# Kernel optimization log

Measured on AMD Instinct MI355X. Metric: run time of the kernel, lower is better.

## Reference

```python
import jax, jax.numpy as jnp
import numpy as np
from jax import lax

# Problem constants (match input_specs / init_kwargs)
B, N, F_IN = 16, 4096, 64          # clouds, points per cloud, feature dim
RATIO, R, K = 0.25, 0.1, 64        # fps ratio, ball radius, max neighbors
S = int(N * RATIO)                 # sampled centers per cloud (1024)
H1, H2, OUT = 64, 64, 128          # MLP [F_IN+3 -> 64 -> 64 -> 128]


def _fps(pos):
    """Farthest point sampling on one cloud. pos: [N,3] -> idx [S] (start at 0)."""
    def step(carry, _):
        mind, last = carry
        d = jnp.sum((pos - pos[last]) ** 2, axis=-1)
        mind = jnp.minimum(mind, d)
        nxt = jnp.argmax(mind)
        return (mind, nxt), nxt
    init = (jnp.full((pos.shape[0],), jnp.inf, pos.dtype), jnp.array(0))
    _, rest = lax.scan(step, init, None, length=S - 1)
    return jnp.concatenate([jnp.zeros((1,), rest.dtype), rest])


def _mlp(h, W1, b1, W2, b2, W3, b3):
    h = jax.nn.relu(h @ W1 + b1)
    h = jax.nn.relu(h @ W2 + b2)
    return jax.nn.relu(h @ W3 + b3)


def setup_inputs() -> dict:
    key = jax.random.key(0)
    ks = jax.random.split(key, 8)
    x = jax.random.normal(ks[0], (B * N, F_IN), jnp.float32)
    pos = jax.random.uniform(ks[1], (B * N, 3), jnp.float32)  # unit cube
    batch = jnp.arange(B * N, dtype=jnp.int64) // N           # cloud ids, equal-size clouds
    d_in = F_IN + 3
    W1 = jax.random.normal(ks[2], (d_in, H1), jnp.float32) / np.sqrt(d_in)
    b1 = jnp.zeros((H1,), jnp.float32)
    W2 = jax.random.normal(ks[3], (H1, H2), jnp.float32) / np.sqrt(H1)
    b2 = jnp.zeros((H2,), jnp.float32)
    W3 = jax.random.normal(ks[4], (H2, OUT), jnp.float32) / np.sqrt(H2)
    b3 = jnp.zeros((OUT,), jnp.float32)
    return {"x": x, "pos": pos, "batch": batch,
            "W1": W1, "b1": b1, "W2": W2, "b2": b2, "W3": W3, "b3": b3}


def reference(x, pos, batch, W1, b1, W2, b2, W3, b3):
    xb = x.reshape(B, N, F_IN)
    pb = pos.reshape(B, N, 3)
    # --- fps(pos, batch, ratio) : per-cloud farthest point sampling ---
    idx = jax.vmap(_fps)(pb)                                   # [B,S]
    pos_s = jnp.take_along_axis(pb, idx[:, :, None], axis=1)   # [B,S,3]
    # --- radius(pos, pos[idx], r, max_num_neighbors=K) : ball query ---
    d2 = jnp.sum((pos_s[:, :, None, :] - pb[:, None, :, :]) ** 2, axis=-1)  # [B,S,N]
    neg = jnp.where(d2 <= R * R, -d2, -jnp.inf)
    vals, nbr = lax.top_k(neg, K)                              # [B,S,K] nearest-in-ball
    valid = jnp.isfinite(vals)                                 # center is its own neighbor -> >=1 valid
    # --- PointNetConv: msg = nn(concat(x_j, pos_j - pos_i)), max aggregation ---
    x_j = jax.vmap(lambda a, i: a[i])(xb, nbr)                 # [B,S,K,F_IN]
    p_j = jax.vmap(lambda a, i: a[i])(pb, nbr)                 # [B,S,K,3]
    msg = jnp.concatenate([x_j, p_j - pos_s[:, :, None, :]], axis=-1)
    m = _mlp(msg, W1, b1, W2, b2, W3, b3)                      # [B,S,K,OUT]
    m = jnp.where(valid[..., None], m, -jnp.inf)
    out = jnp.max(m, axis=2)                                   # [B,S,OUT]
    batch_s = jnp.take_along_axis(batch.reshape(B, N), idx, axis=1).reshape(-1)
    return out.reshape(B * S, OUT), pos_s.reshape(B * S, 3), batch_s
```

## Files before the change

kernel.cpp:

```cpp
#include <hip/hip_runtime.h>
#include <hip/hip_bf16.h>
#include <math.h>


#define NB 16
#define NP 4096
#define FIN 64
#define NS 1024
#define KN 64
#define CAP 256
#define CPB 8

typedef __attribute__((ext_vector_type(8))) short bf16x8;
typedef __attribute__((ext_vector_type(4))) float f32x4;

__device__ __forceinline__ float dist2e(float ax, float ay, float az,
                                        float bx, float by, float bz) {
    float dx = __fsub_rn(ax, bx);
    float dy = __fsub_rn(ay, by);
    float dz = __fsub_rn(az, bz);
    return __fadd_rn(__fadd_rn(__fmul_rn(dx, dx), __fmul_rn(dy, dy)),
                     __fmul_rn(dz, dz));
}

__device__ __forceinline__ short f2bf(float f) {
    unsigned u = __float_as_uint(f);
    unsigned r = (u + 0x7FFFu + ((u >> 16) & 1u)) >> 16;
    return (short)r;
}

#define DPP_KEY_MAX(k, CTRL)                                                   \
    do {                                                                       \
        int _lo = (int)(unsigned)((k) & 0xFFFFFFFFull);                        \
        int _hi = (int)(unsigned)((k) >> 32);                                  \
        int _plo = __builtin_amdgcn_update_dpp(_lo, _lo, CTRL, 0xF, 0xF, false);\
        int _phi = __builtin_amdgcn_update_dpp(_hi, _hi, CTRL, 0xF, 0xF, false);\
        unsigned long long _nk =                                               \
            ((unsigned long long)(unsigned)_phi << 32) | (unsigned)_plo;       \
        if (_nk > (k)) (k) = _nk;                                              \
    } while (0)

__global__ __launch_bounds__(256) void fps_kernel(const float* __restrict__ pos,
                                                  int* __restrict__ fps_idx,
                                                  float* __restrict__ out_pos,
                                                  float* __restrict__ out_batch) {
    const int b = blockIdx.x;
    const int tid = threadIdx.x;
    const int wv = tid >> 6;
    __shared__ __align__(16) float4 hist[NS];
    __shared__ __align__(16) float bc[2][4][8];
    const float* p = pos + (size_t)b * NP * 3;
    float lx[16], ly[16], lz[16], md[16];
#pragma unroll
    for (int i = 0; i < 16; ++i) {
        int j = tid + (i << 8);
        lx[i] = p[j * 3 + 0];
        ly[i] = p[j * 3 + 1];
        lz[i] = p[j * 3 + 2];
        md[i] = INFINITY;
    }
    const float c0x = p[0], c0y = p[1], c0z = p[2];
    float cx = c0x, cy = c0y, cz = c0z;
    for (int s = 1; s < NS; ++s) {
        float bv = -1.0f;
        int bi = 0;
        float wx = 0.f, wy = 0.f, wz = 0.f;
#pragma unroll
        for (int i = 0; i < 16; ++i) {
            float d = dist2e(lx[i], ly[i], lz[i], cx, cy, cz);
            float m = md[i];
            m = d < m ? d : m;
            md[i] = m;
            bool take = (m > bv);
            bv = take ? m : bv;
            bi = take ? (tid + (i << 8)) : bi;
            wx = take ? lx[i] : wx;
            wy = take ? ly[i] : wy;
            wz = take ? lz[i] : wz;
        }
        unsigned long long key =
            ((unsigned long long)__float_as_uint(bv) << 32) |
            (unsigned)(~(unsigned)bi);
        const unsigned long long my = key;
        DPP_KEY_MAX(key, 0x111);
        DPP_KEY_MAX(key, 0x112);
        DPP_KEY_MAX(key, 0x114);
        DPP_KEY_MAX(key, 0x118);
        DPP_KEY_MAX(key, 0x142);
        DPP_KEY_MAX(key, 0x143);
        const unsigned kwlo =
            (unsigned)__builtin_amdgcn_readlane((int)(unsigned)(key & 0xFFFFFFFFull), 63);
        const unsigned kwhi =
            (unsigned)__builtin_amdgcn_readlane((int)(unsigned)(key >> 32), 63);
        const unsigned long long kw = ((unsigned long long)kwhi << 32) | kwlo;
        const int buf = s & 1;
        if (my == kw) {
            bc[buf][wv][0] = __uint_as_float(kwlo);
            bc[buf][wv][1] = __uint_as_float(kwhi);
            bc[buf][wv][2] = wx;
            bc[buf][wv][3] = wy;
            bc[buf][wv][4] = wz;
        }
        __syncthreads();
        unsigned long long bk;
        float bx, by, bz;
        {
            float4 e = *(const float4*)&bc[buf][0][0];
            bk = ((unsigned long long)__float_as_uint(e.y) << 32) |
                 __float_as_uint(e.x);
            bx = e.z; by = e.w; bz = bc[buf][0][4];
        }
#pragma unroll
        for (int w = 1; w < 4; ++w) {
            float4 e = *(const float4*)&bc[buf][w][0];
            unsigned long long k2 =
                ((unsigned long long)__float_as_uint(e.y) << 32) |
                __float_as_uint(e.x);
            float z2 = bc[buf][w][4];
            bool take = (k2 > bk);
            bk = take ? k2 : bk;
            bx = take ? e.z : bx;
            by = take ? e.w : by;
            bz = take ? z2 : bz;
        }
        const int cur = (int)(~(unsigned)(bk & 0xFFFFFFFFull));
        cx = bx; cy = by; cz = bz;
        if (tid == 0) hist[s] = make_float4(__int_as_float(cur), bx, by, bz);
    }
    __syncthreads();
    for (int s = tid; s < NS; s += 256) {
        if (s == 0) {
            fps_idx[b * NS] = 0;
            out_pos[(size_t)(b * NS) * 3 + 0] = c0x;
            out_pos[(size_t)(b * NS) * 3 + 1] = c0y;
            out_pos[(size_t)(b * NS) * 3 + 2] = c0z;
        } else {
            float4 e = hist[s];
            fps_idx[b * NS + s] = __float_as_int(e.x);
            out_pos[(size_t)(b * NS + s) * 3 + 0] = e.y;
            out_pos[(size_t)(b * NS + s) * 3 + 1] = e.z;
            out_pos[(size_t)(b * NS + s) * 3 + 2] = e.w;
        }
        out_batch[b * NS + s] = (float)b;
    }
}

__global__ __launch_bounds__(256) void ball_kernel(const float* __restrict__ pos,
                                                   const int* __restrict__ fps_idx,
                                                   int* __restrict__ nbr_cnt,
                                                   int* __restrict__ nbr_idx) {
    __shared__ float px[NP], py[NP], pz[NP];
    __shared__ float cd2[4][CAP];
    __shared__ int cix[4][CAP];
    const int tid = threadIdx.x;
    const int wv = tid >> 6, lane = tid & 63;
    const int b = blockIdx.x >> 4;
    const int grp = blockIdx.x & 15;
    const float* p = pos + (size_t)b * NP * 3;
    for (int e = tid; e < NP; e += 256) {
        px[e] = p[e * 3 + 0];
        py[e] = p[e * 3 + 1];
        pz[e] = p[e * 3 + 2];
    }
    __syncthreads();
    for (int i = 0; i < 16; ++i) {
        const int s = grp * 64 + i * 4 + wv;
        const int cen = b * NS + s;
        const int ci = fps_idx[cen];
        const float cx = px[ci], cy = py[ci], cz = pz[ci];
        int cnt = 0;
        for (int it = 0; it < NP / 64; ++it) {
            const int j = it * 64 + lane;
            float d2 = dist2e(cx, cy, cz, px[j], py[j], pz[j]);
            bool in = (d2 <= 0.01f);
            unsigned long long m = __ballot(in);
            if (in) {
                int slot = cnt + __popcll(m & ((1ull << lane) - 1ull));
                if (slot < CAP) { cd2[wv][slot] = d2; cix[wv][slot] = j; }
            }
            cnt += __popcll(m);
        }
        if (cnt > CAP) cnt = CAP;
        const int keep = cnt <= KN ? cnt : KN;
        if (lane == 0) nbr_cnt[cen] = keep;
        if (cnt <= KN) {
            if (lane < cnt) nbr_idx[(size_t)cen * KN + lane] = cix[wv][lane];
        } else {
            for (int e = lane; e < cnt; e += 64) {
                float d = cd2[wv][e];
                int id = cix[wv][e];
                int rank = 0;
                for (int q = 0; q < cnt; ++q) {
                    float dq = cd2[wv][q];
                    int iq = cix[wv][q];
                    rank += (dq < d || (dq == d && iq < id)) ? 1 : 0;
                }
                if (rank < KN) nbr_idx[(size_t)cen * KN + rank] = id;
            }
        }
    }
}

__global__ __launch_bounds__(256) void conv_kernel(const float* __restrict__ pos,
                                                   const float* __restrict__ x,
                                                   const int* __restrict__ fps_idx,
                                                   const int* __restrict__ nbr_cnt,
                                                   const int* __restrict__ nbr_idx,
                                                   const float* __restrict__ W1,
                                                   const float* __restrict__ b1,
                                                   const float* __restrict__ W2,
                                                   const float* __restrict__ b2,
                                                   const float* __restrict__ W3,
                                                   const float* __restrict__ b3,
                                                   float* __restrict__ out) {
    const int tid = threadIdx.x;
    const int lane = tid & 63;
    const int w = tid >> 6;
    const int lg = lane >> 4;
    const int lr = lane & 15;
    __shared__ short h1s[64 * 64];
    __shared__ short h2s[64 * 64];
    __shared__ float dpx[64], dpy[64], dpz[64];
    __shared__ int jr[64];
    __shared__ float omax[4][128];
    bf16x8 w1f[3][4], w2f[2][4], w3f[2][8];
#pragma unroll
    for (int kt = 0; kt < 3; ++kt)
#pragma unroll
        for (int ct = 0; ct < 4; ++ct) {
            bf16x8 f;
#pragma unroll
            for (int i = 0; i < 8; ++i) {
                int k = 32 * kt + 8 * lg + i;
                float v = (k < 67) ? W1[k * 64 + 16 * ct + lr] : 0.f;
                f[i] = f2bf(v);
            }
            w1f[kt][ct] = f;
        }
#pragma unroll
    for (int kt = 0; kt < 2; ++kt)
#pragma unroll
        for (int ct = 0; ct < 4; ++ct) {
            bf16x8 f;
#pragma unroll
            for (int i = 0; i < 8; ++i) {
                int k = 32 * kt + 8 * lg + i;
                f[i] = f2bf(W2[k * 64 + 16 * ct + lr]);
            }
            w2f[kt][ct] = f;
        }
#pragma unroll
    for (int kt = 0; kt < 2; ++kt)
#pragma unroll
        for (int ct = 0; ct < 8; ++ct) {
            bf16x8 f;
#pragma unroll
            for (int i = 0; i < 8; ++i) {
                int k = 32 * kt + 8 * lg + i;
                f[i] = f2bf(W3[k * 128 + 16 * ct + lr]);
            }
            w3f[kt][ct] = f;
        }
    float b1v[4], b2v[4], b3v[8];
#pragma unroll
    for (int ct = 0; ct < 4; ++ct) { b1v[ct] = b1[16 * ct + lr]; b2v[ct] = b2[16 * ct + lr]; }
#pragma unroll
    for (int ct = 0; ct < 8; ++ct) b3v[ct] = b3[16 * ct + lr];

    for (int cc = 0; cc < CPB; ++cc) {
        const int cen = blockIdx.x * CPB + cc;
        const int b = cen >> 10;
        const int C = nbr_cnt[cen];
        if (tid < 64) {
            const float* pb = pos + (size_t)b * NP * 3;
            const int ci = fps_idx[cen];
            const float cx = pb[ci * 3 + 0], cy = pb[ci * 3 + 1], cz = pb[ci * 3 + 2];
            if (tid < C) {
                int j = nbr_idx[(size_t)cen * KN + tid];
                jr[tid] = b * NP + j;
                dpx[tid] = pb[j * 3 + 0] - cx;
                dpy[tid] = pb[j * 3 + 1] - cy;
                dpz[tid] = pb[j * 3 + 2] - cz;
            } else {
                jr[tid] = b * NP;
                dpx[tid] = 0.f; dpy[tid] = 0.f; dpz[tid] = 0.f;
            }
        }
        __syncthreads();
        const int arow = 16 * w + lr;
        bf16x8 a0, a1, a2;
        {
            const float* xr = x + (size_t)jr[arow] * FIN + 8 * lg;
            float4 v0 = *(const float4*)(xr + 0);
            float4 v1 = *(const float4*)(xr + 4);
            float4 v2 = *(const float4*)(xr + 32);
            float4 v3 = *(const float4*)(xr + 36);
            a0[0] = f2bf(v0.x); a0[1] = f2bf(v0.y); a0[2] = f2bf(v0.z); a0[3] = f2bf(v0.w);
            a0[4] = f2bf(v1.x); a0[5] = f2bf(v1.y); a0[6] = f2bf(v1.z); a0[7] = f2bf(v1.w);
            a1[0] = f2bf(v2.x); a1[1] = f2bf(v2.y); a1[2] = f2bf(v2.z); a1[3] = f2bf(v2.w);
            a1[4] = f2bf(v3.x); a1[5] = f2bf(v3.y); a1[6] = f2bf(v3.z); a1[7] = f2bf(v3.w);
            float d0 = (lg == 0) ? dpx[arow] : 0.f;
            float d1 = (lg == 0) ? dpy[arow] : 0.f;
            float d2 = (lg == 0) ? dpz[arow] : 0.f;
            a2[0] = f2bf(d0); a2[1] = f2bf(d1); a2[2] = f2bf(d2);
            a2[3] = 0; a2[4] = 0; a2[5] = 0; a2[6] = 0; a2[7] = 0;
        }
        {
            f32x4 acc[4];
#pragma unroll
            for (int ct = 0; ct < 4; ++ct) {
                acc[ct] = (f32x4){b1v[ct], b1v[ct], b1v[ct], b1v[ct]};
                acc[ct] = __builtin_amdgcn_mfma_f32_16x16x32_bf16(a0, w1f[0][ct], acc[ct], 0, 0, 0);
                acc[ct] = __builtin_amdgcn_mfma_f32_16x16x32_bf16(a1, w1f[1][ct], acc[ct], 0, 0, 0);
                acc[ct] = __builtin_amdgcn_mfma_f32_16x16x32_bf16(a2, w1f[2][ct], acc[ct], 0, 0, 0);
            }
#pragma unroll
            for (int ct = 0; ct < 4; ++ct)
#pragma unroll
                for (int r = 0; r < 4; ++r) {
                    int rw = 16 * w + 4 * lg + r;
                    int idx = rw * 64 + 16 * ct + lr;
                    h1s[idx ^ ((rw & 7) << 3)] = f2bf(fmaxf(acc[ct][r], 0.f));
                }
        }
        bf16x8 ha0 = *(bf16x8*)&h1s[(arow * 64 + 0  + 8 * lg) ^ ((arow & 7) << 3)];
        bf16x8 ha1 = *(bf16x8*)&h1s[(arow * 64 + 32 + 8 * lg) ^ ((arow & 7) << 3)];
        {
            f32x4 acc[4];
#pragma unroll
            for (int ct = 0; ct < 4; ++ct) {
                acc[ct] = (f32x4){b2v[ct], b2v[ct], b2v[ct], b2v[ct]};
                acc[ct] = __builtin_amdgcn_mfma_f32_16x16x32_bf16(ha0, w2f[0][ct], acc[ct], 0, 0, 0);
                acc[ct] = __builtin_amdgcn_mfma_f32_16x16x32_bf16(ha1, w2f[1][ct], acc[ct], 0, 0, 0);
            }
#pragma unroll
            for (int ct = 0; ct < 4; ++ct)
#pragma unroll
                for (int r = 0; r < 4; ++r) {
                    int rw = 16 * w + 4 * lg + r;
                    int idx = rw * 64 + 16 * ct + lr;
                    h2s[idx ^ ((rw & 7) << 3)] = f2bf(fmaxf(acc[ct][r], 0.f));
                }
        }
        bf16x8 hb0 = *(bf16x8*)&h2s[(arow * 64 + 0  + 8 * lg) ^ ((arow & 7) << 3)];
        bf16x8 hb1 = *(bf16x8*)&h2s[(arow * 64 + 32 + 8 * lg) ^ ((arow & 7) << 3)];
        {
            f32x4 acc3[8];
#pragma unroll
            for (int ct = 0; ct < 8; ++ct) {
                acc3[ct] = (f32x4){b3v[ct], b3v[ct], b3v[ct], b3v[ct]};
                acc3[ct] = __builtin_amdgcn_mfma_f32_16x16x32_bf16(hb0, w3f[0][ct], acc3[ct], 0, 0, 0);
                acc3[ct] = __builtin_amdgcn_mfma_f32_16x16x32_bf16(hb1, w3f[1][ct], acc3[ct], 0, 0, 0);
            }
#pragma unroll
            for (int ct = 0; ct < 8; ++ct) {
                float m = -INFINITY;
#pragma unroll
                for (int r = 0; r < 4; ++r) {
                    int rg = 16 * w + 4 * lg + r;
                    float v = fmaxf(acc3[ct][r], 0.f);
                    m = (rg < C && v > m) ? v : m;
                }
                m = fmaxf(m, __shfl_xor(m, 16, 64));
                m = fmaxf(m, __shfl_xor(m, 32, 64));
                if (lg == 0) omax[w][16 * ct + lr] = m;
            }
        }
        __syncthreads();
        if (tid < 128) {
            float m = fmaxf(fmaxf(omax[0][tid], omax[1][tid]),
                            fmaxf(omax[2][tid], omax[3][tid]));
            out[(size_t)cen * 128 + tid] = m;
        }
        __syncthreads();
    }
}

extern "C" void kernel_launch(void* const* d_in, const int* in_sizes, int n_in,
                              void* d_out, int out_size, void* d_ws, size_t ws_size,
                              hipStream_t stream) {
    const float* x   = (const float*)d_in[0];
    const float* pos = (const float*)d_in[1];
    const float* W1  = (const float*)d_in[3];
    const float* b1  = (const float*)d_in[4];
    const float* W2  = (const float*)d_in[5];
    const float* b2  = (const float*)d_in[6];
    const float* W3  = (const float*)d_in[7];
    const float* b3  = (const float*)d_in[8];
    float* out = (float*)d_out;
    char* ws = (char*)d_ws;
    int* fps_idx = (int*)(ws);
    int* nbr_cnt = (int*)(ws + 16384 * 4);
    int* nbr_idx = (int*)(ws + 16384 * 8);
    float* out_feat  = out;
    float* out_pos   = out + (size_t)16384 * 128;
    float* out_batch = out + (size_t)16384 * 131;
    fps_kernel<<<NB, 256, 0, stream>>>(pos, fps_idx, out_pos, out_batch);
    ball_kernel<<<NB * 16, 256, 0, stream>>>(pos, fps_idx, nbr_cnt, nbr_idx);
    conv_kernel<<<NB * NS / CPB, 256, 0, stream>>>(pos, x, fps_idx, nbr_cnt,
                                                   nbr_idx, W1, b1, W2, b2,
                                                   W3, b3, out_feat);
}
```

Measured before the change: 1.141 ms.

## Fuse FPS, ball query and conv into one persistent kernel with progress flags

Replaces the three sequential kernels with one persistent launch. Sixteen blocks run farthest point sampling and publish sampled centers to global memory every 64 steps behind a release/acquire progress counter. The other 240 blocks spin on those counters and do the ball query and MLP max-aggregation for centers already produced, so neighbor search and convolution overlap the serial FPS. This relies on all 256 blocks being co-resident, adds spin-wait and fence overhead, and lowers the candidate cap to 128 while reading positions from global memory instead of shared memory.

```diff
diff --git a/kernel.cpp b/kernel.cpp
--- a/kernel.cpp
+++ b/kernel.cpp
@@ -8,8 +8,9 @@
 #define FIN 64
 #define NS 1024
 #define KN 64
-#define CAP 256
-#define CPB 8
+#define CAP 128
+#define NCONS 240
+#define NCHUNK 4096
 
 typedef __attribute__((ext_vector_type(8))) short bf16x8;
 typedef __attribute__((ext_vector_type(4))) float f32x4;
@@ -40,339 +41,361 @@
         if (_nk > (k)) (k) = _nk;                                              \
     } while (0)
 
-__global__ __launch_bounds__(256) void fps_kernel(const float* __restrict__ pos,
-                                                  int* __restrict__ fps_idx,
-                                                  float* __restrict__ out_pos,
-                                                  float* __restrict__ out_batch) {
-    const int b = blockIdx.x;
+#define SMEM_BYTES 27648
+
+__global__ __launch_bounds__(256) void fused_kernel(
+        const float* __restrict__ pos, const float* __restrict__ x,
+        const float* __restrict__ W1, const float* __restrict__ b1,
+        const float* __restrict__ W2, const float* __restrict__ b2,
+        const float* __restrict__ W3, const float* __restrict__ b3,
+        float* __restrict__ out_feat, float* __restrict__ out_pos,
+        float* __restrict__ out_batch, float* __restrict__ histg,
+        int* __restrict__ progress) {
+    __shared__ __align__(16) char smem[SMEM_BYTES];
     const int tid = threadIdx.x;
+    const int lane = tid & 63;
     const int wv = tid >> 6;
-    __shared__ __align__(16) float4 hist[NS];
-    __shared__ __align__(16) float bc[2][4][8];
-    const float* p = pos + (size_t)b * NP * 3;
-    float lx[16], ly[16], lz[16], md[16];
-#pragma unroll
-    for (int i = 0; i < 16; ++i) {
-        int j = tid + (i << 8);
-        lx[i] = p[j * 3 + 0];
-        ly[i] = p[j * 3 + 1];
-        lz[i] = p[j * 3 + 2];
-        md[i] = INFINITY;
-    }
-    const float c0x = p[0], c0y = p[1], c0z = p[2];
-    float cx = c0x, cy = c0y, cz = c0z;
-    for (int s = 1; s < NS; ++s) {
-        float bv = -1.0f;
-        int bi = 0;
-        float wx = 0.f, wy = 0.f, wz = 0.f;
+
+    if (blockIdx.x < NB) {
+        const int b = blockIdx.x;
+        float4* hist = (float4*)smem;
+        float (*bc)[4][8] = (float(*)[4][8])(smem + 16384);
+        const float* p = pos + (size_t)b * NP * 3;
+        float lx[16], ly[16], lz[16], md[16];
 #pragma unroll
         for (int i = 0; i < 16; ++i) {
-            float d = dist2e(lx[i], ly[i], lz[i], cx, cy, cz);
-            float m = md[i];
-            m = d < m ? d : m;
-            md[i] = m;
-            bool take = (m > bv);
-            bv = take ? m : bv;
-            bi = take ? (tid + (i << 8)) : bi;
-            wx = take ? lx[i] : wx;
-            wy = take ? ly[i] : wy;
-            wz = take ? lz[i] : wz;
-        }
-        unsigned long long key =
-            ((unsigned long long)__float_as_uint(bv) << 32) |
-            (unsigned)(~(unsigned)bi);
-        const unsigned long long my = key;
-        DPP_KEY_MAX(key, 0x111);
-        DPP_KEY_MAX(key, 0x112);
-        DPP_KEY_MAX(key, 0x114);
-        DPP_KEY_MAX(key, 0x118);
-        DPP_KEY_MAX(key, 0x142);
-        DPP_KEY_MAX(key, 0x143);
-        const unsigned kwlo =
-            (unsigned)__builtin_amdgcn_readlane((int)(unsigned)(key & 0xFFFFFFFFull), 63);
-        const unsigned kwhi =
-            (unsigned)__builtin_amdgcn_readlane((int)(unsigned)(key >> 32), 63);
-        const unsigned long long kw = ((unsigned long long)kwhi << 32) | kwlo;
-        const int buf = s & 1;
-        if (my == kw) {
-            bc[buf][wv][0] = __uint_as_float(kwlo);
-            bc[buf][wv][1] = __uint_as_float(kwhi);
-            bc[buf][wv][2] = wx;
-            bc[buf][wv][3] = wy;
-            bc[buf][wv][4] = wz;
+            int j = tid + (i << 8);
+            lx[i] = p[j * 3 + 0];
+            ly[i] = p[j * 3 + 1];
+            lz[i] = p[j * 3 + 2];
+            md[i] = INFINITY;
+        }
+        const float c0x = p[0], c0y = p[1], c0z = p[2];
+        float cx = c0x, cy = c0y, cz = c0z;
+        if (tid == 0) hist[0] = make_float4(0.f, c0x, c0y, c0z);
+        for (int s = 1; s < NS; ++s) {
+            float bv = -1.0f;
+            int bi = 0;
+            float wx = 0.f, wy = 0.f, wz = 0.f;
+#pragma unroll
+            for (int i = 0; i < 16; ++i) {
+                float d = dist2e(lx[i], ly[i], lz[i], cx, cy, cz);
+                float m = md[i];
+                m = d < m ? d : m;
+                md[i] = m;
+                bool take = (m > bv);
+                bv = take ? m : bv;
+                bi = take ? (tid + (i << 8)) : bi;
+                wx = take ? lx[i] : wx;
+                wy = take ? ly[i] : wy;
+                wz = take ? lz[i] : wz;
+            }
+            unsigned long long key =
+                ((unsigned long long)__float_as_uint(bv) << 32) |
+                (unsigned)(~(unsigned)bi);
+            const unsigned long long my = key;
+            DPP_KEY_MAX(key, 0x111);
+            DPP_KEY_MAX(key, 0x112);
+            DPP_KEY_MAX(key, 0x114);
+            DPP_KEY_MAX(key, 0x118);
+            DPP_KEY_MAX(key, 0x142);
+            DPP_KEY_MAX(key, 0x143);
+            const unsigned kwlo = (unsigned)__builtin_amdgcn_readlane(
+                (int)(unsigned)(key & 0xFFFFFFFFull), 63);
+            const unsigned kwhi = (unsigned)__builtin_amdgcn_readlane(
+                (int)(unsigned)(key >> 32), 63);
+            const unsigned long long kw =
+                ((unsigned long long)kwhi << 32) | kwlo;
+            const int buf = s & 1;
+            if (my == kw) {
+                bc[buf][wv][0] = __uint_as_float(kwlo);
+                bc[buf][wv][1] = __uint_as_float(kwhi);
+                bc[buf][wv][2] = wx;
+                bc[buf][wv][3] = wy;
+                bc[buf][wv][4] = wz;
+            }
+            __syncthreads();
+            if ((s & 63) == 0) {
+                const int base = s - 64;
+                if (tid < 192) {
+                    int cc = tid / 3, comp = tid % 3;
+                    float4 h = hist[base + cc];
+                    float v = comp == 0 ? h.y : (comp == 1 ? h.z : h.w);
+                    __hip_atomic_store(
+                        (unsigned*)&histg[((size_t)(b * NS + base + cc)) * 3 + comp],
+                        __float_as_uint(v), __ATOMIC_RELAXED,
+                        __HIP_MEMORY_SCOPE_AGENT);
+                }
+                __threadfence();
+                __syncthreads();
+                if (tid == 0)
+                    __hip_atomic_store(&progress[b], s, __ATOMIC_RELEASE,
+                                       __HIP_MEMORY_SCOPE_AGENT);
+            }
+            unsigned long long bk;
+            float bx, by, bz;
+            {
+                float4 e = *(const float4*)&bc[buf][0][0];
+                bk = ((unsigned long long)__float_as_uint(e.y) << 32) |
+                     __float_as_uint(e.x);
+                bx = e.z; by = e.w; bz = bc[buf][0][4];
+            }
+#pragma unroll
+            for (int w = 1; w < 4; ++w) {
+                float4 e = *(const float4*)&bc[buf][w][0];
+                unsigned long long k2 =
+                    ((unsigned long long)__float_as_uint(e.y) << 32) |
+                    __float_as_uint(e.x);
+                float z2 = bc[buf][w][4];
+                bool take = (k2 > bk);
+                bk = take ? k2 : bk;
+                bx = take ? e.z : bx;
+                by = take ? e.w : by;
+                bz = take ? z2 : bz;
+            }
+            const int cur = (int)(~(unsigned)(bk & 0xFFFFFFFFull));
+            cx = bx; cy = by; cz = bz;
+            if (tid == 0)
+                hist[s] = make_float4(__int_as_float(cur), bx, by, bz);
         }
         __syncthreads();
-        unsigned long long bk;
-        float bx, by, bz;
-        {
-            float4 e = *(const float4*)&bc[buf][0][0];
-            bk = ((unsigned long long)__float_as_uint(e.y) << 32) |
-                 __float_as_uint(e.x);
-            bx = e.z; by = e.w; bz = bc[buf][0][4];
-        }
-#pragma unroll
-        for (int w = 1; w < 4; ++w) {
-            float4 e = *(const float4*)&bc[buf][w][0];
-            unsigned long long k2 =
-                ((unsigned long long)__float_as_uint(e.y) << 32) |
-                __float_as_uint(e.x);
-            float z2 = bc[buf][w][4];
-            bool take = (k2 > bk);
-            bk = take ? k2 : bk;
-            bx = take ? e.z : bx;
-            by = take ? e.w : by;
-            bz = take ? z2 : bz;
-        }
-        const int cur = (int)(~(unsigned)(bk & 0xFFFFFFFFull));
-        cx = bx; cy = by; cz = bz;
-        if (tid == 0) hist[s] = make_float4(__int_as_float(cur), bx, by, bz);
-    }
-    __syncthreads();
-    for (int s = tid; s < NS; s += 256) {
-        if (s == 0) {
-            fps_idx[b * NS] = 0;
-            out_pos[(size_t)(b * NS) * 3 + 0] = c0x;
-            out_pos[(size_t)(b * NS) * 3 + 1] = c0y;
-            out_pos[(size_t)(b * NS) * 3 + 2] = c0z;
-        } else {
+        if (tid < 192) {
+            int cc = tid / 3, comp = tid % 3;
+            float4 h = hist[960 + cc];
+            float v = comp == 0 ? h.y : (comp == 1 ? h.z : h.w);
+            __hip_atomic_store(
+                (unsigned*)&histg[((size_t)(b * NS + 960 + cc)) * 3 + comp],
+                __float_as_uint(v), __ATOMIC_RELAXED, __HIP_MEMORY_SCOPE_AGENT);
+        }
+        __threadfence();
+        __syncthreads();
+        if (tid == 0)
+            __hip_atomic_store(&progress[b], NS, __ATOMIC_RELEASE,
+                               __HIP_MEMORY_SCOPE_AGENT);
+        for (int s = tid; s < NS; s += 256) {
             float4 e = hist[s];
-            fps_idx[b * NS + s] = __float_as_int(e.x);
             out_pos[(size_t)(b * NS + s) * 3 + 0] = e.y;
             out_pos[(size_t)(b * NS + s) * 3 + 1] = e.z;
             out_pos[(size_t)(b * NS + s) * 3 + 2] = e.w;
-        }
-        out_batch[b * NS + s] = (float)b;
+            out_batch[b * NS + s] = (float)b;
+        }
+        return;
     }
-}
-
-__global__ __launch_bounds__(256) void ball_kernel(const float* __restrict__ pos,
-                                                   const int* __restrict__ fps_idx,
-                                                   int* __restrict__ nbr_cnt,
-                                                   int* __restrict__ nbr_idx) {
-    __shared__ float px[NP], py[NP], pz[NP];
-    __shared__ float cd2[4][CAP];
-    __shared__ int cix[4][CAP];
-    const int tid = threadIdx.x;
-    const int wv = tid >> 6, lane = tid & 63;
-    const int b = blockIdx.x >> 4;
-    const int grp = blockIdx.x & 15;
-    const float* p = pos + (size_t)b * NP * 3;
-    for (int e = tid; e < NP; e += 256) {
-        px[e] = p[e * 3 + 0];
-        py[e] = p[e * 3 + 1];
-        pz[e] = p[e * 3 + 2];
+
+    const int w = blockIdx.x - NB;
+    short* h1s = (short*)smem;
+    short* h2s = (short*)(smem + 8192);
+    float* cd2 = (float*)(smem + 16384);
+    int*   cix = (int*)(smem + 18432);
+    float* dpxA = (float*)(smem + 20480);
+    float* dpyA = (float*)(smem + 21504);
+    float* dpzA = (float*)(smem + 22528);
+    int*   jA   = (int*)(smem + 23552);
+    float* omax = (float*)(smem + 24576);
+    int*   keepW = (int*)(smem + 26624);
+    const int lg = lane >> 4;
+    const int lr = lane & 15;
+    bf16x8 w1f[3][4], w2f[2][4], w3f[2][8];
+#pragma unroll
+    for (int kt = 0; kt < 3; ++kt)
+#pragma unroll
+        for (int ct = 0; ct < 4; ++ct) {
+            bf16x8 f;
+#pragma unroll
+            for (int i = 0; i < 8; ++i) {
+                int k = 32 * kt + 8 * lg + i;
+                float v = (k < 67) ? W1[k * 64 + 16 * ct + lr] : 0.f;
+                f[i] = f2bf(v);
+            }
+            w1f[kt][ct] = f;
+        }
+#pragma unroll
+    for (int kt = 0; kt < 2; ++kt)
+#pragma unroll
+        for (int ct = 0; ct < 4; ++ct) {
+            bf16x8 f;
+#pragma unroll
+            for (int i = 0; i < 8; ++i) {
+                int k = 32 * kt + 8 * lg + i;
+                f[i] = f2bf(W2[k * 64 + 16 * ct + lr]);
+            }
+            w2f[kt][ct] = f;
+        }
+#pragma unroll
+    for (int kt = 0; kt < 2; ++kt)
+#pragma unroll
+        for (int ct = 0; ct < 8; ++ct) {
+            bf16x8 f;
+#pragma unroll
+            for (int i = 0; i < 8; ++i) {
+                int k = 32 * kt + 8 * lg + i;
+                f[i] = f2bf(W3[k * 128 + 16 * ct + lr]);
+            }
+            w3f[kt][ct] = f;
+        }
+    float b1v[4], b2v[4], b3v[8];
+#pragma unroll
+    for (int ct = 0; ct < 4; ++ct) {
+        b1v[ct] = b1[16 * ct + lr];
+        b2v[ct] = b2[16 * ct + lr];
     }
-    __syncthreads();
-    for (int i = 0; i < 16; ++i) {
-        const int s = grp * 64 + i * 4 + wv;
-        const int cen = b * NS + s;
-        const int ci = fps_idx[cen];
-        const float cx = px[ci], cy = py[ci], cz = pz[ci];
+#pragma unroll
+    for (int ct = 0; ct < 8; ++ct) b3v[ct] = b3[16 * ct + lr];
+
+    for (int c = w; c < NCHUNK; c += NCONS) {
+        const int s = c >> 2;
+        const int bq = (c & 3) << 2;
+        const int bw = bq + wv;
+        while (__hip_atomic_load(&progress[bw], __ATOMIC_ACQUIRE,
+                                 __HIP_MEMORY_SCOPE_AGENT) <= s) {
+            __builtin_amdgcn_s_sleep(2);
+        }
+        const size_t ho = ((size_t)(bw * NS + s)) * 3;
+        const float ccx = __uint_as_float(__hip_atomic_load(
+            (const unsigned*)&histg[ho + 0], __ATOMIC_RELAXED,
+            __HIP_MEMORY_SCOPE_AGENT));
+        const float ccy = __uint_as_float(__hip_atomic_load(
+            (const unsigned*)&histg[ho + 1], __ATOMIC_RELAXED,
+            __HIP_MEMORY_SCOPE_AGENT));
+        const float ccz = __uint_as_float(__hip_atomic_load(
+            (const unsigned*)&histg[ho + 2], __ATOMIC_RELAXED,
+            __HIP_MEMORY_SCOPE_AGENT));
         int cnt = 0;
-        for (int it = 0; it < NP / 64; ++it) {
+        const float* pcloud = pos + (size_t)bw * NP * 3;
+        for (int it = 0; it < 64; ++it) {
             const int j = it * 64 + lane;
-            float d2 = dist2e(cx, cy, cz, px[j], py[j], pz[j]);
+            const float* pp = pcloud + (size_t)j * 3;
+            float d2 = dist2e(ccx, ccy, ccz, pp[0], pp[1], pp[2]);
             bool in = (d2 <= 0.01f);
             unsigned long long m = __ballot(in);
             if (in) {
                 int slot = cnt + __popcll(m & ((1ull << lane) - 1ull));
-                if (slot < CAP) { cd2[wv][slot] = d2; cix[wv][slot] = j; }
+                if (slot < CAP) {
+                    cd2[wv * CAP + slot] = d2;
+                    cix[wv * CAP + slot] = j;
+                }
             }
             cnt += __popcll(m);
         }
         if (cnt > CAP) cnt = CAP;
         const int keep = cnt <= KN ? cnt : KN;
-        if (lane == 0) nbr_cnt[cen] = keep;
+        if (lane == 0) keepW[wv] = keep;
+        jA[wv * 64 + lane] = 0;
         if (cnt <= KN) {
-            if (lane < cnt) nbr_idx[(size_t)cen * KN + lane] = cix[wv][lane];
+            if (lane < keep) jA[wv * 64 + lane] = cix[wv * CAP + lane];
         } else {
             for (int e = lane; e < cnt; e += 64) {
-                float d = cd2[wv][e];
-                int id = cix[wv][e];
+                float d = cd2[wv * CAP + e];
+                int id = cix[wv * CAP + e];
                 int rank = 0;
                 for (int q = 0; q < cnt; ++q) {
-                    float dq = cd2[wv][q];
-                    int iq = cix[wv][q];
+                    float dq = cd2[wv * CAP + q];
+                    int iq = cix[wv * CAP + q];
                     rank += (dq < d || (dq == d && iq < id)) ? 1 : 0;
                 }
-                if (rank < KN) nbr_idx[(size_t)cen * KN + rank] = id;
-            }
-        }
-    }
-}
-
-__global__ __launch_bounds__(256) void conv_kernel(const float* __restrict__ pos,
-                                                   const float* __restrict__ x,
-                                                   const int* __restrict__ fps_idx,
-                                                   const int* __restrict__ nbr_cnt,
-                                                   const int* __restrict__ nbr_idx,
-                                                   const float* __restrict__ W1,
-                                                   const float* __restrict__ b1,
-                                                   const float* __restrict__ W2,
-                                                   const float* __restrict__ b2,
-                                                   const float* __restrict__ W3,
-                                                   const float* __restrict__ b3,
-                                                   float* __restrict__ out) {
-    const int tid = threadIdx.x;
-    const int lane = tid & 63;
-    const int w = tid >> 6;
-    const int lg = lane >> 4;
-    const int lr = lane & 15;
-    __shared__ short h1s[64 * 64];
-    __shared__ short h2s[64 * 64];
-    __shared__ float dpx[64], dpy[64], dpz[64];
-    __shared__ int jr[64];
-    __shared__ float omax[4][128];
-    bf16x8 w1f[3][4], w2f[2][4], w3f[2][8];
-#pragma unroll
-    for (int kt = 0; kt < 3; ++kt)
-#pragma unroll
-        for (int ct = 0; ct < 4; ++ct) {
-            bf16x8 f;
-#pragma unroll
-            for (int i = 0; i < 8; ++i) {
-                int k = 32 * kt + 8 * lg + i;
-                float v = (k < 67) ? W1[k * 64 + 16 * ct + lr] : 0.f;
-                f[i] = f2bf(v);
-            }
-            w1f[kt][ct] = f;
-        }
-#pragma unroll
-    for (int kt = 0; kt < 2; ++kt)
-#pragma unroll
-        for (int ct = 0; ct < 4; ++ct) {
-            bf16x8 f;
-#pragma unroll
-            for (int i = 0; i < 8; ++i) {
-                int k = 32 * kt + 8 * lg + i;
-                f[i] = f2bf(W2[k * 64 + 16 * ct + lr]);
-            }
-            w2f[kt][ct] = f;
-        }
-#pragma unroll
-    for (int kt = 0; kt < 2; ++kt)
-#pragma unroll
-        for (int ct = 0; ct < 8; ++ct) {
-            bf16x8 f;
-#pragma unroll
-            for (int i = 0; i < 8; ++i) {
-                int k = 32 * kt + 8 * lg + i;
-                f[i] = f2bf(W3[k * 128 + 16 * ct + lr]);
-            }
-            w3f[kt][ct] = f;
-        }
-    float b1v[4], b2v[4], b3v[8];
-#pragma unroll
-    for (int ct = 0; ct < 4; ++ct) { b1v[ct] = b1[16 * ct + lr]; b2v[ct] = b2[16 * ct + lr]; }
-#pragma unroll
-    for (int ct = 0; ct < 8; ++ct) b3v[ct] = b3[16 * ct + lr];
-
-    for (int cc = 0; cc < CPB; ++cc) {
-        const int cen = blockIdx.x * CPB + cc;
-        const int b = cen >> 10;
-        const int C = nbr_cnt[cen];
-        if (tid < 64) {
-            const float* pb = pos + (size_t)b * NP * 3;
-            const int ci = fps_idx[cen];
-            const float cx = pb[ci * 3 + 0], cy = pb[ci * 3 + 1], cz = pb[ci * 3 + 2];
-            if (tid < C) {
-                int j = nbr_idx[(size_t)cen * KN + tid];
-                jr[tid] = b * NP + j;
-                dpx[tid] = pb[j * 3 + 0] - cx;
-                dpy[tid] = pb[j * 3 + 1] - cy;
-                dpz[tid] = pb[j * 3 + 2] - cz;
-            } else {
-                jr[tid] = b * NP;
-                dpx[tid] = 0.f; dpy[tid] = 0.f; dpz[tid] = 0.f;
-            }
+                if (rank < KN) jA[wv * 64 + rank] = id;
+            }
+        }
+        {
+            int j = jA[wv * 64 + lane];
+            const float* pp = pcloud + (size_t)j * 3;
+            bool valid = lane < keep;
+            dpxA[wv * 64 + lane] = valid ? (pp[0] - ccx) : 0.f;
+            dpyA[wv * 64 + lane] = valid ? (pp[1] - ccy) : 0.f;
+            dpzA[wv * 64 + lane] = valid ? (pp[2] - ccz) : 0.f;
         }
         __syncthreads();
-        const int arow = 16 * w + lr;
-        bf16x8 a0, a1, a2;
-        {
-            const float* xr = x + (size_t)jr[arow] * FIN + 8 * lg;
-            float4 v0 = *(const float4*)(xr + 0);
-            float4 v1 = *(const float4*)(xr + 4);
-            float4 v2 = *(const float4*)(xr + 32);
-            float4 v3 = *(const float4*)(xr + 36);
-            a0[0] = f2bf(v0.x); a0[1] = f2bf(v0.y); a0[2] = f2bf(v0.z); a0[3] = f2bf(v0.w);
-            a0[4] = f2bf(v1.x); a0[5] = f2bf(v1.y); a0[6] = f2bf(v1.z); a0[7] = f2bf(v1.w);
-            a1[0] = f2bf(v2.x); a1[1] = f2bf(v2.y); a1[2] = f2bf(v2.z); a1[3] = f2bf(v2.w);
-            a1[4] = f2bf(v3.x); a1[5] = f2bf(v3.y); a1[6] = f2bf(v3.z); a1[7] = f2bf(v3.w);
-            float d0 = (lg == 0) ? dpx[arow] : 0.f;
-            float d1 = (lg == 0) ? dpy[arow] : 0.f;
-            float d2 = (lg == 0) ? dpz[arow] : 0.f;
-            a2[0] = f2bf(d0); a2[1] = f2bf(d1); a2[2] = f2bf(d2);
-            a2[3] = 0; a2[4] = 0; a2[5] = 0; a2[6] = 0; a2[7] = 0;
-        }
-        {
-            f32x4 acc[4];
-#pragma unroll
-            for (int ct = 0; ct < 4; ++ct) {
-                acc[ct] = (f32x4){b1v[ct], b1v[ct], b1v[ct], b1v[ct]};
-                acc[ct] = __builtin_amdgcn_mfma_f32_16x16x32_bf16(a0, w1f[0][ct], acc[ct], 0, 0, 0);
-                acc[ct] = __builtin_amdgcn_mfma_f32_16x16x32_bf16(a1, w1f[1][ct], acc[ct], 0, 0, 0);
-                acc[ct] = __builtin_amdgcn_mfma_f32_16x16x32_bf16(a2, w1f[2][ct], acc[ct], 0, 0, 0);
-            }
-#pragma unroll
-            for (int ct = 0; ct < 4; ++ct)
-#pragma unroll
-                for (int r = 0; r < 4; ++r) {
-                    int rw = 16 * w + 4 * lg + r;
-                    int idx = rw * 64 + 16 * ct + lr;
-                    h1s[idx ^ ((rw & 7) << 3)] = f2bf(fmaxf(acc[ct][r], 0.f));
-                }
-        }
-        bf16x8 ha0 = *(bf16x8*)&h1s[(arow * 64 + 0  + 8 * lg) ^ ((arow & 7) << 3)];
-        bf16x8 ha1 = *(bf16x8*)&h1s[(arow * 64 + 32 + 8 * lg) ^ ((arow & 7) << 3)];
-        {
-            f32x4 acc[4];
-#pragma unroll
-            for (int ct = 0; ct < 4; ++ct) {
-                acc[ct] = (f32x4){b2v[ct], b2v[ct], b2v[ct], b2v[ct]};
-                acc[ct] = __builtin_amdgcn_mfma_f32_16x16x32_bf16(ha0, w2f[0][ct], acc[ct], 0, 0, 0);
-                acc[ct] = __builtin_amdgcn_mfma_f32_16x16x32_bf16(ha1, w2f[1][ct], acc[ct], 0, 0, 0);
-            }
-#pragma unroll
-            for (int ct = 0; ct < 4; ++ct)
-#pragma unroll
-                for (int r = 0; r < 4; ++r) {
-                    int rw = 16 * w + 4 * lg + r;
-                    int idx = rw * 64 + 16 * ct + lr;
-                    h2s[idx ^ ((rw & 7) << 3)] = f2bf(fmaxf(acc[ct][r], 0.f));
-                }
-        }
-        bf16x8 hb0 = *(bf16x8*)&h2s[(arow * 64 + 0  + 8 * lg) ^ ((arow & 7) << 3)];
-        bf16x8 hb1 = *(bf16x8*)&h2s[(arow * 64 + 32 + 8 * lg) ^ ((arow & 7) << 3)];
-        {
-            f32x4 acc3[8];
-#pragma unroll
-            for (int ct = 0; ct < 8; ++ct) {
-                acc3[ct] = (f32x4){b3v[ct], b3v[ct], b3v[ct], b3v[ct]};
-                acc3[ct] = __builtin_amdgcn_mfma_f32_16x16x32_bf16(hb0, w3f[0][ct], acc3[ct], 0, 0, 0);
-                acc3[ct] = __builtin_amdgcn_mfma_f32_16x16x32_bf16(hb1, w3f[1][ct], acc3[ct], 0, 0, 0);
-            }
-#pragma unroll
-            for (int ct = 0; ct < 8; ++ct) {
-                float m = -INFINITY;
-#pragma unroll
-                for (int r = 0; r < 4; ++r) {
-                    int rg = 16 * w + 4 * lg + r;
-                    float v = fmaxf(acc3[ct][r], 0.f);
-                    m = (rg < C && v > m) ? v : m;
-                }
-                m = fmaxf(m, __shfl_xor(m, 16, 64));
-                m = fmaxf(m, __shfl_xor(m, 32, 64));
-                if (lg == 0) omax[w][16 * ct + lr] = m;
-            }
-        }
-        __syncthreads();
-        if (tid < 128) {
-            float m = fmaxf(fmaxf(omax[0][tid], omax[1][tid]),
-                            fmaxf(omax[2][tid], omax[3][tid]));
-            out[(size_t)cen * 128 + tid] = m;
-        }
-        __syncthreads();
+        for (int cc = 0; cc < 4; ++cc) {
+            const int C = keepW[cc];
+            const int cen = (bq + cc) * NS + s;
+            const int arow = 16 * wv + lr;
+            bf16x8 a0, a1, a2;
+            {
+                const int jrow = (bq + cc) * NP + jA[cc * 64 + arow];
+                const float* xr = x + (size_t)jrow * FIN + 8 * lg;
+                float4 v0 = *(const float4*)(xr + 0);
+                float4 v1 = *(const float4*)(xr + 4);
+                float4 v2 = *(const float4*)(xr + 32);
+                float4 v3 = *(const float4*)(xr + 36);
+                a0[0] = f2bf(v0.x); a0[1] = f2bf(v0.y); a0[2] = f2bf(v0.z); a0[3] = f2bf(v0.w);
+                a0[4] = f2bf(v1.x); a0[5] = f2bf(v1.y); a0[6] = f2bf(v1.z); a0[7] = f2bf(v1.w);
+                a1[0] = f2bf(v2.x); a1[1] = f2bf(v2.y); a1[2] = f2bf(v2.z); a1[3] = f2bf(v2.w);
+                a1[4] = f2bf(v3.x); a1[5] = f2bf(v3.y); a1[6] = f2bf(v3.z); a1[7] = f2bf(v3.w);
+                float d0 = (lg == 0) ? dpxA[cc * 64 + arow] : 0.f;
+                float d1 = (lg == 0) ? dpyA[cc * 64 + arow] : 0.f;
+                float d2v = (lg == 0) ? dpzA[cc * 64 + arow] : 0.f;
+                a2[0] = f2bf(d0); a2[1] = f2bf(d1); a2[2] = f2bf(d2v);
+                a2[3] = 0; a2[4] = 0; a2[5] = 0; a2[6] = 0; a2[7] = 0;
+            }
+            {
+                f32x4 acc[4];
+#pragma unroll
+                for (int ct = 0; ct < 4; ++ct) {
+                    acc[ct] = (f32x4){b1v[ct], b1v[ct], b1v[ct], b1v[ct]};
+                    acc[ct] = __builtin_amdgcn_mfma_f32_16x16x32_bf16(a0, w1f[0][ct], acc[ct], 0, 0, 0);
+                    acc[ct] = __builtin_amdgcn_mfma_f32_16x16x32_bf16(a1, w1f[1][ct], acc[ct], 0, 0, 0);
+                    acc[ct] = __builtin_amdgcn_mfma_f32_16x16x32_bf16(a2, w1f[2][ct], acc[ct], 0, 0, 0);
+                }
+#pragma unroll
+                for (int ct = 0; ct < 4; ++ct)
+#pragma unroll
+                    for (int r = 0; r < 4; ++r) {
+                        int rw = 16 * wv + 4 * lg + r;
+                        int idx = rw * 64 + 16 * ct + lr;
+                        h1s[idx ^ ((rw & 7) << 3)] = f2bf(fmaxf(acc[ct][r], 0.f));
+                    }
+            }
+            bf16x8 ha0 = *(bf16x8*)&h1s[(arow * 64 + 0  + 8 * lg) ^ ((arow & 7) << 3)];
+            bf16x8 ha1 = *(bf16x8*)&h1s[(arow * 64 + 32 + 8 * lg) ^ ((arow & 7) << 3)];
+            {
+                f32x4 acc[4];
+#pragma unroll
+                for (int ct = 0; ct < 4; ++ct) {
+                    acc[ct] = (f32x4){b2v[ct], b2v[ct], b2v[ct], b2v[ct]};
+                    acc[ct] = __builtin_amdgcn_mfma_f32_16x16x32_bf16(ha0, w2f[0][ct], acc[ct], 0, 0, 0);
+                    acc[ct] = __builtin_amdgcn_mfma_f32_16x16x32_bf16(ha1, w2f[1][ct], acc[ct], 0, 0, 0);
+                }
+#pragma unroll
+                for (int ct = 0; ct < 4; ++ct)
+#pragma unroll
+                    for (int r = 0; r < 4; ++r) {
+                        int rw = 16 * wv + 4 * lg + r;
+                        int idx = rw * 64 + 16 * ct + lr;
+                        h2s[idx ^ ((rw & 7) << 3)] = f2bf(fmaxf(acc[ct][r], 0.f));
+                    }
+            }
+            bf16x8 hb0 = *(bf16x8*)&h2s[(arow * 64 + 0  + 8 * lg) ^ ((arow & 7) << 3)];
+            bf16x8 hb1 = *(bf16x8*)&h2s[(arow * 64 + 32 + 8 * lg) ^ ((arow & 7) << 3)];
+            {
+                f32x4 acc3[8];
+#pragma unroll
+                for (int ct = 0; ct < 8; ++ct) {
+                    acc3[ct] = (f32x4){b3v[ct], b3v[ct], b3v[ct], b3v[ct]};
+                    acc3[ct] = __builtin_amdgcn_mfma_f32_16x16x32_bf16(hb0, w3f[0][ct], acc3[ct], 0, 0, 0);
+                    acc3[ct] = __builtin_amdgcn_mfma_f32_16x16x32_bf16(hb1, w3f[1][ct], acc3[ct], 0, 0, 0);
+                }
+#pragma unroll
+                for (int ct = 0; ct < 8; ++ct) {
+                    float m = -INFINITY;
+#pragma unroll
+                    for (int r = 0; r < 4; ++r) {
+                        int rg = 16 * wv + 4 * lg + r;
+                        float v = fmaxf(acc3[ct][r], 0.f);
+                        m = (rg < C && v > m) ? v : m;
+                    }
+                    m = fmaxf(m, __shfl_xor(m, 16, 64));
+                    m = fmaxf(m, __shfl_xor(m, 32, 64));
+                    if (lg == 0) omax[wv * 128 + 16 * ct + lr] = m;
+                }
+            }
+            __syncthreads();
+            if (tid < 128) {
+                float m = fmaxf(fmaxf(omax[0 * 128 + tid], omax[1 * 128 + tid]),
+                                fmaxf(omax[2 * 128 + tid], omax[3 * 128 + tid]));
+                out_feat[(size_t)cen * 128 + tid] = m;
+            }
+            __syncthreads();
+        }
     }
 }
 
@@ -389,15 +412,13 @@
     const float* b3  = (const float*)d_in[8];
     float* out = (float*)d_out;
     char* ws = (char*)d_ws;
-    int* fps_idx = (int*)(ws);
-    int* nbr_cnt = (int*)(ws + 16384 * 4);
-    int* nbr_idx = (int*)(ws + 16384 * 8);
+    int*   progress = (int*)ws;
+    float* histg    = (float*)(ws + 256);
     float* out_feat  = out;
     float* out_pos   = out + (size_t)16384 * 128;
     float* out_batch = out + (size_t)16384 * 131;
-    fps_kernel<<<NB, 256, 0, stream>>>(pos, fps_idx, out_pos, out_batch);
-    ball_kernel<<<NB * 16, 256, 0, stream>>>(pos, fps_idx, nbr_cnt, nbr_idx);
-    conv_kernel<<<NB * NS / CPB, 256, 0, stream>>>(pos, x, fps_idx, nbr_cnt,
-                                                   nbr_idx, W1, b1, W2, b2,
-                                                   W3, b3, out_feat);
+    hipMemsetAsync(ws, 0, 256, stream);
+    fused_kernel<<<256, 256, 0, stream>>>(pos, x, W1, b1, W2, b2, W3, b3,
+                                          out_feat, out_pos, out_batch,
+                                          histg, progress);
 }
```

Result: faster. 960.7 us (-15.8%).
